# Kernel optimization log

Hardware: AMD Instinct MI355X
Metric: run time of the kernel (lower is better)

The kernel has to match this reference:

```python
import jax, jax.numpy as jnp
import numpy as np

B, C, H, W = 32, 3, 480, 640
_GRAY_W = jnp.array([0.299, 0.587, 0.114], dtype=jnp.float32)  # torchvision rgb_to_grayscale weights


def _blend(img1, img2, ratio):
    # torchvision _blend for float images: clamp to [0, 1]
    return jnp.clip(ratio * img1 + (1.0 - ratio) * img2, 0.0, 1.0)


def _rgb_to_gray(x):
    # x: [B,3,H,W] -> [B,1,H,W]
    return jnp.einsum('bchw,c->bhw', x, _GRAY_W)[:, None]


def _adjust_hue(x, hf):
    # x: [B,3,H,W] in [0,1], hf: [B] hue shift. RGB->HSV, h += hf (mod 1), HSV->RGB.
    r, g, b = x[:, 0], x[:, 1], x[:, 2]
    maxc = jnp.max(x, axis=1)
    minc = jnp.min(x, axis=1)
    v = maxc
    cr = maxc - minc
    eqc = cr == 0
    crd = jnp.where(eqc, 1.0, cr)
    s = cr / jnp.where(maxc == 0, 1.0, maxc)
    rc = (maxc - r) / crd
    gc = (maxc - g) / crd
    bc = (maxc - b) / crd
    hr = jnp.where(maxc == r, bc - gc, 0.0)
    hg = jnp.where((maxc == g) & (maxc != r), 2.0 + rc - bc, 0.0)
    hb = jnp.where((maxc != g) & (maxc != r), 4.0 + gc - rc, 0.0)
    h = ((hr + hg + hb) / 6.0) % 1.0
    h = (h + hf[:, None, None]) % 1.0
    # HSV -> RGB
    i6 = h * 6.0
    i = jnp.floor(i6)
    f = i6 - i
    i = i.astype(jnp.int32) % 6
    p = v * (1.0 - s)
    q = v * (1.0 - f * s)
    t = v * (1.0 - (1.0 - f) * s)

    def sel(a0, a1, a2, a3, a4, a5):
        return jnp.select([i == 0, i == 1, i == 2, i == 3, i == 4], [a0, a1, a2, a3, a4], a5)

    r2 = sel(v, q, p, p, t, v)
    g2 = sel(t, v, v, q, p, p)
    b2 = sel(p, p, t, v, v, q)
    return jnp.stack([r2, g2, b2], axis=1)


def setup_inputs() -> dict:
    key = jax.random.key(0)
    k0, k1, k2, k3, k4 = jax.random.split(key, 5)
    x = jax.random.uniform(k0, (B, C, H, W), dtype=jnp.float32)
    brightness_f = jax.random.uniform(k1, (B,), minval=0.7, maxval=1.3, dtype=jnp.float32)
    contrast_f = jax.random.uniform(k2, (B,), minval=0.7, maxval=1.3, dtype=jnp.float32)
    saturation_f = jax.random.uniform(k3, (B,), minval=0.7, maxval=1.3, dtype=jnp.float32)
    hue_f = jax.random.uniform(k4, (B,), minval=-0.3, maxval=0.3, dtype=jnp.float32)
    return {"x": x, "brightness_f": brightness_f, "contrast_f": contrast_f,
            "saturation_f": saturation_f, "hue_f": hue_f, "num_samples": 1}


def reference(x, brightness_f, contrast_f, saturation_f, hue_f, num_samples):
    # Replicate each image num_samples times along batch -> [B*N, 3, H, W]
    x = jnp.repeat(x, num_samples, axis=0)
    bf = brightness_f[:, None, None, None]
    cf = contrast_f[:, None, None, None]
    sf = saturation_f[:, None, None, None]
    # brightness: blend with zeros
    x = jnp.clip(x * bf, 0.0, 1.0)
    # contrast: blend with per-image mean of grayscale
    gray = _rgb_to_gray(x)
    mean = jnp.mean(gray, axis=(2, 3), keepdims=True)
    x = _blend(x, mean, cf)
    # saturation: blend with grayscale of current image
    x = _blend(x, _rgb_to_gray(x), sf)
    # hue shift via HSV roundtrip
    x = _adjust_hue(x, hue_f)
    return x
```

## Files before the change

kernel.cpp:

```cpp
#include <hip/hip_runtime.h>

#define HW      307200
#define HW4     76800
#define CHW     921600
#define RED_BPB 60
#define APP_BPB 300

typedef float vfloat4 __attribute__((ext_vector_type(4)));

struct RGB { float r, g, b; };

__global__ __launch_bounds__(256) void cr_reduce_gray(
    const float* __restrict__ x,
    const float* __restrict__ bright,
    float* __restrict__ part_ws,
    int ns)
{
    int b   = blockIdx.x / RED_BPB;
    int blk = blockIdx.x % RED_BPB;
    int b_in = (ns == 1) ? b : (b / ns);

    const vfloat4* rp = (const vfloat4*)(x + (size_t)b_in * CHW);
    const vfloat4* gp = rp + HW4;
    const vfloat4* bp = gp + HW4;
    float bf = bright[b];

    float acc = 0.0f;
    #pragma unroll
    for (int it = 0; it < 5; ++it) {
        int p = blk * 256 + threadIdx.x + it * (RED_BPB * 256);
        vfloat4 r  = rp[p];
        vfloat4 g  = gp[p];
        vfloat4 bl = bp[p];
        #pragma unroll
        for (int k = 0; k < 4; ++k) {
            float rr = fminf(fmaxf(r[k]  * bf, 0.0f), 1.0f);
            float gg = fminf(fmaxf(g[k]  * bf, 0.0f), 1.0f);
            float bb = fminf(fmaxf(bl[k] * bf, 0.0f), 1.0f);
            acc += 0.299f * rr + 0.587f * gg + 0.114f * bb;
        }
    }

    #pragma unroll
    for (int off = 32; off > 0; off >>= 1)
        acc += __shfl_down(acc, off);

    __shared__ float wsum[4];
    int lane = threadIdx.x & 63;
    int wave = threadIdx.x >> 6;
    if (lane == 0) wsum[wave] = acc;
    __syncthreads();
    if (threadIdx.x == 0)
        part_ws[b * RED_BPB + blk] = wsum[0] + wsum[1] + wsum[2] + wsum[3];
}

__device__ __forceinline__ RGB cr_process(
    float r, float g, float b,
    float bf, float cf, float sf, float hf, float cmean)
{
    r = fminf(fmaxf(r * bf, 0.0f), 1.0f);
    g = fminf(fmaxf(g * bf, 0.0f), 1.0f);
    b = fminf(fmaxf(b * bf, 0.0f), 1.0f);
    r = fminf(fmaxf(cf * r + cmean, 0.0f), 1.0f);
    g = fminf(fmaxf(cf * g + cmean, 0.0f), 1.0f);
    b = fminf(fmaxf(cf * b + cmean, 0.0f), 1.0f);
    float gray = 0.299f * r + 0.587f * g + 0.114f * b;
    float oms = (1.0f - sf) * gray;
    r = fminf(fmaxf(sf * r + oms, 0.0f), 1.0f);
    g = fminf(fmaxf(sf * g + oms, 0.0f), 1.0f);
    b = fminf(fmaxf(sf * b + oms, 0.0f), 1.0f);

    float maxc = fmaxf(r, fmaxf(g, b));
    float minc = fminf(r, fminf(g, b));
    float v  = maxc;
    float cr = maxc - minc;
    float crd = (cr == 0.0f) ? 1.0f : cr;
    float invcrd = 1.0f / crd;
    float md = (maxc == 0.0f) ? 1.0f : maxc;
    float s = cr / md;
    float rc = (maxc - r) * invcrd;
    float gc = (maxc - g) * invcrd;
    float bc = (maxc - b) * invcrd;

    float h = (maxc == r) ? (bc - gc)
            : ((maxc == g) ? (2.0f + rc - bc)
                           : (4.0f + gc - rc));
    h = h * (1.0f / 6.0f);
    h = h - floorf(h);
    h = h + hf;
    h = h - floorf(h);

    float i6 = h * 6.0f;
    float fi = floorf(i6);
    float f  = i6 - fi;
    int i = ((int)fi) % 6;

    float p = v * (1.0f - s);
    float q = v * (1.0f - f * s);
    float t = v * (1.0f - (1.0f - f) * s);

    RGB o;
    o.r = (i == 0 || i == 5) ? v : (i == 1 ? q : (i == 4 ? t : p));
    o.g = (i == 1 || i == 2) ? v : (i == 0 ? t : (i == 3 ? q : p));
    o.b = (i == 3 || i == 4) ? v : (i == 5 ? q : (i == 2 ? t : p));
    return o;
}

__global__ __launch_bounds__(256) void cr_apply(
    const float* __restrict__ x,
    const float* __restrict__ bright,
    const float* __restrict__ contrast,
    const float* __restrict__ sat,
    const float* __restrict__ hue,
    const float* __restrict__ part_ws,
    float* __restrict__ out,
    int ns)
{
    int b    = blockIdx.x / APP_BPB;
    int pblk = blockIdx.x % APP_BPB;
    int p4   = pblk * 256 + threadIdx.x;
    int b_in = (ns == 1) ? b : (b / ns);

    __shared__ float smean;
    if (threadIdx.x < 64) {
        float v = (threadIdx.x < RED_BPB) ? part_ws[b * RED_BPB + threadIdx.x] : 0.0f;
        #pragma unroll
        for (int off = 32; off > 0; off >>= 1)
            v += __shfl_down(v, off);
        if (threadIdx.x == 0) smean = v * (1.0f / (float)HW);
    }
    __syncthreads();

    const vfloat4* rp = (const vfloat4*)(x + (size_t)b_in * CHW);
    const vfloat4* gp = rp + HW4;
    const vfloat4* bp = gp + HW4;
    vfloat4* orp = (vfloat4*)(out + (size_t)b * CHW);
    vfloat4* ogp = orp + HW4;
    vfloat4* obp = ogp + HW4;

    float bf = bright[b];
    float cf = contrast[b];
    float sf = sat[b];
    float hf = hue[b];
    float cmean = (1.0f - cf) * smean;

    vfloat4 r  = rp[p4];
    vfloat4 g  = gp[p4];
    vfloat4 bl = bp[p4];
    vfloat4 ro, go, bo;

    #pragma unroll
    for (int k = 0; k < 4; ++k) {
        RGB o = cr_process(r[k], g[k], bl[k], bf, cf, sf, hf, cmean);
        ro[k] = o.r;
        go[k] = o.g;
        bo[k] = o.b;
    }

    __builtin_nontemporal_store(ro, &orp[p4]);
    __builtin_nontemporal_store(go, &ogp[p4]);
    __builtin_nontemporal_store(bo, &obp[p4]);
}

extern "C" void kernel_launch(void* const* d_in, const int* in_sizes, int n_in,
                              void* d_out, int out_size, void* d_ws, size_t ws_size,
                              hipStream_t stream) {
    const float* x  = (const float*)d_in[0];
    const float* bf = (const float*)d_in[1];
    const float* cf = (const float*)d_in[2];
    const float* sf = (const float*)d_in[3];
    const float* hf = (const float*)d_in[4];
    float* out = (float*)d_out;

    int ns = out_size / in_sizes[0];
    if (ns < 1) ns = 1;
    int B_out = out_size / CHW;

    float* part_ws = (float*)d_ws;

    cr_reduce_gray<<<dim3(B_out * RED_BPB), dim3(256), 0, stream>>>(
        x, bf, part_ws, ns);

    cr_apply<<<dim3(B_out * APP_BPB), dim3(256), 0, stream>>>(
        x, bf, cf, sf, hf, part_ws, out, ns);
}
```

Measured before the change: 226.3 us.

## Fuse reduction and apply into one cooperative kernel with grid sync

Replaces the two-kernel reduce-then-apply pipeline with a single cooperative kernel. Each block first computes partial grayscale sums over its strided pixels, then waits at a grid-wide barrier before re-reading the input to apply the color transforms. The aim is to remove the second launch and the launch gap, and possibly to hit cache on the second read. The cost is a grid barrier, and a fixed grid of 1024 blocks limits parallelism. If the cooperative launch fails, it falls back to the old two-kernel path.

```diff
diff --git a/kernel.cpp b/kernel.cpp
--- a/kernel.cpp
+++ b/kernel.cpp
@@ -1,58 +1,18 @@
 #include <hip/hip_runtime.h>
+#include <hip/hip_cooperative_groups.h>
 
 #define HW      307200
 #define HW4     76800
 #define CHW     921600
 #define RED_BPB 60
 #define APP_BPB 300
+#define COOP_GRID 1024
+
+namespace cg = cooperative_groups;
 
 typedef float vfloat4 __attribute__((ext_vector_type(4)));
 
 struct RGB { float r, g, b; };
-
-__global__ __launch_bounds__(256) void cr_reduce_gray(
-    const float* __restrict__ x,
-    const float* __restrict__ bright,
-    float* __restrict__ part_ws,
-    int ns)
-{
-    int b   = blockIdx.x / RED_BPB;
-    int blk = blockIdx.x % RED_BPB;
-    int b_in = (ns == 1) ? b : (b / ns);
-
-    const vfloat4* rp = (const vfloat4*)(x + (size_t)b_in * CHW);
-    const vfloat4* gp = rp + HW4;
-    const vfloat4* bp = gp + HW4;
-    float bf = bright[b];
-
-    float acc = 0.0f;
-    #pragma unroll
-    for (int it = 0; it < 5; ++it) {
-        int p = blk * 256 + threadIdx.x + it * (RED_BPB * 256);
-        vfloat4 r  = rp[p];
-        vfloat4 g  = gp[p];
-        vfloat4 bl = bp[p];
-        #pragma unroll
-        for (int k = 0; k < 4; ++k) {
-            float rr = fminf(fmaxf(r[k]  * bf, 0.0f), 1.0f);
-            float gg = fminf(fmaxf(g[k]  * bf, 0.0f), 1.0f);
-            float bb = fminf(fmaxf(bl[k] * bf, 0.0f), 1.0f);
-            acc += 0.299f * rr + 0.587f * gg + 0.114f * bb;
-        }
-    }
-
-    #pragma unroll
-    for (int off = 32; off > 0; off >>= 1)
-        acc += __shfl_down(acc, off);
-
-    __shared__ float wsum[4];
-    int lane = threadIdx.x & 63;
-    int wave = threadIdx.x >> 6;
-    if (lane == 0) wsum[wave] = acc;
-    __syncthreads();
-    if (threadIdx.x == 0)
-        part_ws[b * RED_BPB + blk] = wsum[0] + wsum[1] + wsum[2] + wsum[3];
-}
 
 __device__ __forceinline__ RGB cr_process(
     float r, float g, float b,
@@ -106,6 +66,139 @@
     return o;
 }
 
+__global__ __launch_bounds__(256, 4) void cr_fused(
+    const float* __restrict__ x,
+    const float* __restrict__ bright,
+    const float* __restrict__ contrast,
+    const float* __restrict__ sat,
+    const float* __restrict__ hue,
+    float* __restrict__ part_ws,
+    float* __restrict__ out,
+    int ns, int bpb)
+{
+    int b   = blockIdx.x / bpb;
+    int blk = blockIdx.x % bpb;
+    int b_in = (ns == 1) ? b : (b / ns);
+
+    const vfloat4* rp = (const vfloat4*)(x + (size_t)b_in * CHW);
+    const vfloat4* gp = rp + HW4;
+    const vfloat4* bp = gp + HW4;
+
+    float bf = bright[b];
+    int stride = bpb * 256;
+    int p0 = blk * 256 + (int)threadIdx.x;
+
+    float acc = 0.0f;
+    for (int p = p0; p < HW4; p += stride) {
+        vfloat4 r  = rp[p];
+        vfloat4 g  = gp[p];
+        vfloat4 bl = bp[p];
+        #pragma unroll
+        for (int k = 0; k < 4; ++k) {
+            float rr = fminf(fmaxf(r[k]  * bf, 0.0f), 1.0f);
+            float gg = fminf(fmaxf(g[k]  * bf, 0.0f), 1.0f);
+            float bb = fminf(fmaxf(bl[k] * bf, 0.0f), 1.0f);
+            acc += 0.299f * rr + 0.587f * gg + 0.114f * bb;
+        }
+    }
+
+    #pragma unroll
+    for (int off = 32; off > 0; off >>= 1)
+        acc += __shfl_down(acc, off);
+
+    __shared__ float wsum[4];
+    int lane = threadIdx.x & 63;
+    int wave = threadIdx.x >> 6;
+    if (lane == 0) wsum[wave] = acc;
+    __syncthreads();
+    if (threadIdx.x == 0)
+        part_ws[b * bpb + blk] = wsum[0] + wsum[1] + wsum[2] + wsum[3];
+
+    cg::this_grid().sync();
+
+    __shared__ float smean;
+    if (threadIdx.x < 64) {
+        float v = 0.0f;
+        for (int i = threadIdx.x; i < bpb; i += 64)
+            v += part_ws[b * bpb + i];
+        #pragma unroll
+        for (int off = 32; off > 0; off >>= 1)
+            v += __shfl_down(v, off);
+        if (threadIdx.x == 0) smean = v * (1.0f / (float)HW);
+    }
+    __syncthreads();
+
+    float cf = contrast[b];
+    float sf = sat[b];
+    float hf = hue[b];
+    float cmean = (1.0f - cf) * smean;
+
+    vfloat4* orp = (vfloat4*)(out + (size_t)b * CHW);
+    vfloat4* ogp = orp + HW4;
+    vfloat4* obp = ogp + HW4;
+
+    for (int p = p0; p < HW4; p += stride) {
+        vfloat4 r  = rp[p];
+        vfloat4 g  = gp[p];
+        vfloat4 bl = bp[p];
+        vfloat4 ro, go, bo;
+        #pragma unroll
+        for (int k = 0; k < 4; ++k) {
+            RGB o = cr_process(r[k], g[k], bl[k], bf, cf, sf, hf, cmean);
+            ro[k] = o.r;
+            go[k] = o.g;
+            bo[k] = o.b;
+        }
+        __builtin_nontemporal_store(ro, &orp[p]);
+        __builtin_nontemporal_store(go, &ogp[p]);
+        __builtin_nontemporal_store(bo, &obp[p]);
+    }
+}
+
+__global__ __launch_bounds__(256) void cr_reduce_gray(
+    const float* __restrict__ x,
+    const float* __restrict__ bright,
+    float* __restrict__ part_ws,
+    int ns)
+{
+    int b   = blockIdx.x / RED_BPB;
+    int blk = blockIdx.x % RED_BPB;
+    int b_in = (ns == 1) ? b : (b / ns);
+
+    const vfloat4* rp = (const vfloat4*)(x + (size_t)b_in * CHW);
+    const vfloat4* gp = rp + HW4;
+    const vfloat4* bp = gp + HW4;
+    float bf = bright[b];
+
+    float acc = 0.0f;
+    #pragma unroll
+    for (int it = 0; it < 5; ++it) {
+        int p = blk * 256 + threadIdx.x + it * (RED_BPB * 256);
+        vfloat4 r  = rp[p];
+        vfloat4 g  = gp[p];
+        vfloat4 bl = bp[p];
+        #pragma unroll
+        for (int k = 0; k < 4; ++k) {
+            float rr = fminf(fmaxf(r[k]  * bf, 0.0f), 1.0f);
+            float gg = fminf(fmaxf(g[k]  * bf, 0.0f), 1.0f);
+            float bb = fminf(fmaxf(bl[k] * bf, 0.0f), 1.0f);
+            acc += 0.299f * rr + 0.587f * gg + 0.114f * bb;
+        }
+    }
+
+    #pragma unroll
+    for (int off = 32; off > 0; off >>= 1)
+        acc += __shfl_down(acc, off);
+
+    __shared__ float wsum[4];
+    int lane = threadIdx.x & 63;
+    int wave = threadIdx.x >> 6;
+    if (lane == 0) wsum[wave] = acc;
+    __syncthreads();
+    if (threadIdx.x == 0)
+        part_ws[b * RED_BPB + blk] = wsum[0] + wsum[1] + wsum[2] + wsum[3];
+}
+
 __global__ __launch_bounds__(256) void cr_apply(
     const float* __restrict__ x,
     const float* __restrict__ bright,
@@ -178,9 +271,25 @@
 
     float* part_ws = (float*)d_ws;
 
-    cr_reduce_gray<<<dim3(B_out * RED_BPB), dim3(256), 0, stream>>>(
-        x, bf, part_ws, ns);
-
-    cr_apply<<<dim3(B_out * APP_BPB), dim3(256), 0, stream>>>(
-        x, bf, cf, sf, hf, part_ws, out, ns);
-}
+    int bpb = COOP_GRID / B_out;
+    if (bpb < 1) bpb = 1;
+
+    bool coop_ok = (B_out * bpb <= COOP_GRID);
+    hipError_t err = hipErrorUnknown;
+    if (coop_ok) {
+        void* args[] = {
+            (void*)&x, (void*)&bf, (void*)&cf, (void*)&sf, (void*)&hf,
+            (void*)&part_ws, (void*)&out, (void*)&ns, (void*)&bpb
+        };
+        err = hipLaunchCooperativeKernel((const void*)cr_fused,
+                                         dim3(B_out * bpb), dim3(256),
+                                         args, 0, stream);
+    }
+
+    if (err != hipSuccess) {
+        cr_reduce_gray<<<dim3(B_out * RED_BPB), dim3(256), 0, stream>>>(
+            x, bf, part_ws, ns);
+        cr_apply<<<dim3(B_out * APP_BPB), dim3(256), 0, stream>>>(
+            x, bf, cf, sf, hf, part_ws, out, ns);
+    }
+}
```

New measurement: 347.1 us. 1.53x slower.
